# Optimization experiments

Hardware: AMD Instinct MI355X
Metric: run time of the kernel (lower is better)

## Reference

```python
import jax, jax.numpy as jnp
import numpy as np

B, H, S, D = 2, 16, 2048, 64

def setup_inputs() -> dict:
    key = jax.random.key(0)
    kq, kk, kv, km, ks = jax.random.split(key, 5)
    return {
        "query_input": jax.random.normal(kq, (B, H, S, D), dtype=jnp.float32),
        "key_input": jax.random.normal(kk, (B, H, S, D), dtype=jnp.float32),
        "value_input": jax.random.normal(kv, (B, H, S, D), dtype=jnp.float32),
        "query_mask": jnp.ones((B, 1, S, 1), dtype=jnp.float32),
        "key_mask": jax.random.uniform(km, (B, 1, 1, S), dtype=jnp.float32),
        "scale_factor": jax.random.normal(ks, (B, 1, 1, 1), dtype=jnp.float32),
        "dropout": 0,
    }

def reference(query_input, key_input, value_input, query_mask, key_mask, scale_factor, dropout):
    # qk = q @ k^T  -> [B, H, S, S]
    qk = jnp.einsum("bhqd,bhkd->bhqk", query_input, key_input)
    scaled_qk = qk * scale_factor                      # elementwise per-batch scale
    softmax_qk = jax.nn.softmax(scaled_qk, axis=-1)
    masked = softmax_qk * key_mask                     # post-softmax multiplicative mask
    # dropout with p=0 is the identity (deterministic baseline)
    output = jnp.einsum("bhqk,bhkd->bhqd", masked, value_input)
    return output
```

## Files before the change

kernel.cpp:

```cpp
#include <hip/hip_runtime.h>
#include <hip/hip_bf16.h>
#include <stdint.h>

#define BB 2
#define HH 16
#define SS 2048
#define DD 64
constexpr int BH = BB * HH;
constexpr int NT = SS / 64;
constexpr int QB = 16;

typedef _Float16 f16_t;
typedef f16_t f16x8 __attribute__((ext_vector_type(8)));
typedef float f32x4 __attribute__((ext_vector_type(4)));

__device__ __forceinline__ uint32_t pkf16(float a, float b) {
    return __builtin_bit_cast(uint32_t, __builtin_amdgcn_cvt_pkrtz(a, b));
}

__global__ __launch_bounds__(256)
void prepack(const float* __restrict__ Kg, const float* __restrict__ Vg,
             const float* __restrict__ Mg, f16_t* __restrict__ Kp,
             f16_t* __restrict__ Vp)
{
    __shared__ float Vs[64][65];
    const int bh = blockIdx.x % BH;
    const int kt = blockIdx.x / BH;
    const int b  = bh / HH;
    const int t  = threadIdx.x;
    const size_t gbase = (size_t)bh * SS * DD + (size_t)kt * 64 * DD;
    const size_t tbase = ((size_t)bh * NT + kt) * 4096;

    for (int c = t; c < 512; c += 256) {
        const int row = c >> 3, j = c & 7;
        const float* kp = Kg + gbase + (size_t)row * DD + j * 8;
        float4 a = *(const float4*)kp;
        float4 d = *(const float4*)(kp + 4);
        uint4 w = make_uint4(pkf16(a.x, a.y), pkf16(a.z, a.w),
                             pkf16(d.x, d.y), pkf16(d.z, d.w));
        *(uint4*)&Kp[tbase + (size_t)row * 64 + ((j ^ (row & 7)) * 8)] = w;
    }

    for (int c = t; c < 1024; c += 256) {
        const int key = c >> 4, dc = (c & 15) * 4;
        float4 v = *(const float4*)(Vg + gbase + (size_t)key * DD + dc);
        const float m = Mg[(size_t)b * SS + kt * 64 + key];
        Vs[key][dc + 0] = v.x * m;
        Vs[key][dc + 1] = v.y * m;
        Vs[key][dc + 2] = v.z * m;
        Vs[key][dc + 3] = v.w * m;
    }
    __syncthreads();

    for (int c = t; c < 512; c += 256) {
        const int dr = c >> 3, j = c & 7;
        float v0 = Vs[j * 8 + 0][dr], v1 = Vs[j * 8 + 1][dr];
        float v2 = Vs[j * 8 + 2][dr], v3 = Vs[j * 8 + 3][dr];
        float v4 = Vs[j * 8 + 4][dr], v5 = Vs[j * 8 + 5][dr];
        float v6 = Vs[j * 8 + 6][dr], v7 = Vs[j * 8 + 7][dr];
        uint4 w = make_uint4(pkf16(v0, v1), pkf16(v2, v3),
                             pkf16(v4, v5), pkf16(v6, v7));
        *(uint4*)&Vp[tbase + (size_t)dr * 64 + ((j ^ (dr & 7)) * 8)] = w;
    }
}

__global__ __launch_bounds__(512)
void fattn8(const float* __restrict__ Qg, const f16_t* __restrict__ Kp,
            const f16_t* __restrict__ Vp, const float* __restrict__ Sg,
            float* __restrict__ Og)
{
    __shared__ __align__(16) f16_t Kt[2][4096];
    __shared__ __align__(16) f16_t Vt[3][4096];
    __shared__ __align__(16) f16_t Pt[8][16][72];

    const int bh   = blockIdx.x % BH;
    const int qt   = blockIdx.x / BH;
    const int b    = bh / HH;
    const int tid  = threadIdx.x;
    const int wave = tid >> 6;
    const int lane = tid & 63;
    const int l16  = lane & 15;
    const int quad = lane >> 4;

    const float sc = Sg[b] * 1.44269504088896340736f;
    const size_t base = (size_t)bh * SS * DD;
    const size_t tb0  = (size_t)bh * NT * 4096;
    const int q0 = qt * 128 + wave * 16;

    auto stage = [&](int kt, int kbuf, int vbuf) {
        const f16_t* ks = Kp + tb0 + (size_t)kt * 4096 + tid * 8;
        const f16_t* vs = Vp + tb0 + (size_t)kt * 4096 + tid * 8;
        __builtin_amdgcn_global_load_lds(
            (const __attribute__((address_space(1))) void*)ks,
            (__attribute__((address_space(3))) void*)&Kt[kbuf][wave * 512],
            16, 0, 0);
        __builtin_amdgcn_global_load_lds(
            (const __attribute__((address_space(1))) void*)vs,
            (__attribute__((address_space(3))) void*)&Vt[vbuf][wave * 512],
            16, 0, 0);
    };

    stage(0, 0, 0);

    f16x8 qf[2];
    {
        const float* qp = Qg + base + (size_t)(q0 + l16) * DD + quad * 8;
#pragma unroll
        for (int kc = 0; kc < 2; ++kc) {
            float4 a  = *(const float4*)(qp + kc * 32);
            float4 b4 = *(const float4*)(qp + kc * 32 + 4);
            f16x8 f;
            f[0] = (f16_t)(a.x * sc);  f[1] = (f16_t)(a.y * sc);
            f[2] = (f16_t)(a.z * sc);  f[3] = (f16_t)(a.w * sc);
            f[4] = (f16_t)(b4.x * sc); f[5] = (f16_t)(b4.y * sc);
            f[6] = (f16_t)(b4.z * sc); f[7] = (f16_t)(b4.w * sc);
            qf[kc] = f;
        }
    }

    f32x4 Ot[4];
#pragma unroll
    for (int mt = 0; mt < 4; ++mt) Ot[mt] = f32x4{0.f, 0.f, 0.f, 0.f};
    float m_run = -1e30f, l_run = 0.0f;

    const int swz = (l16 & 7) << 3;

    int vcur = 0;
    for (int kt = 0; kt < NT; ++kt) {
        const int kcur = kt & 1;
        const int vnxt = (vcur == 2) ? 0 : vcur + 1;
        if (kt + 1 < NT) {
            stage(kt + 1, kcur ^ 1, vnxt);
            asm volatile("s_waitcnt vmcnt(2)" ::: "memory");
        } else {
            asm volatile("s_waitcnt vmcnt(0)" ::: "memory");
        }
        __builtin_amdgcn_s_barrier();

        __builtin_amdgcn_s_setprio(1);
        f32x4 Sfr[4];
#pragma unroll
        for (int mt = 0; mt < 4; ++mt) {
            f32x4 acc = f32x4{0.f, 0.f, 0.f, 0.f};
#pragma unroll
            for (int kc = 0; kc < 2; ++kc) {
                const int off = (mt * 16 + l16) * 64 + ((kc * 32 + quad * 8) ^ swz);
                f16x8 kh = *(const f16x8*)&Kt[kcur][off];
                acc = __builtin_amdgcn_mfma_f32_16x16x32_f16(kh, qf[kc], acc, 0, 0, 0);
            }
            Sfr[mt] = acc;
        }

        if (kt > 0) {
            const int vprv = (vcur == 0) ? 2 : vcur - 1;
#pragma unroll
            for (int kc = 0; kc < 2; ++kc) {
                f16x8 pf = *(const f16x8*)&Pt[wave][l16][kc * 32 + quad * 8];
#pragma unroll
                for (int mt = 0; mt < 4; ++mt) {
                    const int off = (mt * 16 + l16) * 64 + ((kc * 32 + quad * 8) ^ swz);
                    f16x8 vf = *(const f16x8*)&Vt[vprv][off];
                    Ot[mt] = __builtin_amdgcn_mfma_f32_16x16x32_f16(vf, pf, Ot[mt], 0, 0, 0);
                }
            }
        }
        __builtin_amdgcn_s_setprio(0);

        float a0 = fmaxf(fmaxf(Sfr[0][0], Sfr[0][1]), Sfr[0][2]);
        float b0 = fmaxf(fmaxf(Sfr[1][0], Sfr[1][1]), Sfr[1][2]);
        a0 = fmaxf(fmaxf(a0, Sfr[0][3]), Sfr[2][0]);
        b0 = fmaxf(fmaxf(b0, Sfr[1][3]), Sfr[2][1]);
        a0 = fmaxf(fmaxf(a0, Sfr[2][2]), Sfr[3][0]);
        b0 = fmaxf(fmaxf(b0, Sfr[2][3]), Sfr[3][1]);
        a0 = fmaxf(fmaxf(a0, Sfr[3][2]), Sfr[3][3]);
        float mx = fmaxf(a0, b0);
        mx = fmaxf(mx, __shfl_xor(mx, 16));
        mx = fmaxf(mx, __shfl_xor(mx, 32));

        if (__any(mx > m_run + 8.0f)) {
            const float mnew  = fmaxf(m_run, mx);
            const float alpha = __builtin_amdgcn_exp2f(m_run - mnew);
            m_run = mnew;
            l_run *= alpha;
#pragma unroll
            for (int mt = 0; mt < 4; ++mt) Ot[mt] *= alpha;
        }

        float ps[4][4];
#pragma unroll
        for (int mt = 0; mt < 4; ++mt)
#pragma unroll
            for (int r = 0; r < 4; ++r)
                ps[mt][r] = __builtin_amdgcn_exp2f(Sfr[mt][r] - m_run);

        float s0 = (ps[0][0] + ps[0][1]) + (ps[0][2] + ps[0][3]);
        float s1 = (ps[1][0] + ps[1][1]) + (ps[1][2] + ps[1][3]);
        float s2 = (ps[2][0] + ps[2][1]) + (ps[2][2] + ps[2][3]);
        float s3 = (ps[3][0] + ps[3][1]) + (ps[3][2] + ps[3][3]);
        float rs = (s0 + s1) + (s2 + s3);
        rs += __shfl_xor(rs, 16);
        rs += __shfl_xor(rs, 32);
        l_run += rs;

#pragma unroll
        for (int mt = 0; mt < 4; ++mt) {
            uint2 w = make_uint2(pkf16(ps[mt][0], ps[mt][1]),
                                 pkf16(ps[mt][2], ps[mt][3]));
            *(uint2*)&Pt[wave][l16][mt * 16 + quad * 4] = w;
        }

        __builtin_amdgcn_s_barrier();
        vcur = vnxt;
    }

    {
        const int vprv = (vcur == 0) ? 2 : vcur - 1;
#pragma unroll
        for (int kc = 0; kc < 2; ++kc) {
            f16x8 pf = *(const f16x8*)&Pt[wave][l16][kc * 32 + quad * 8];
#pragma unroll
            for (int mt = 0; mt < 4; ++mt) {
                const int off = (mt * 16 + l16) * 64 + ((kc * 32 + quad * 8) ^ swz);
                f16x8 vf = *(const f16x8*)&Vt[vprv][off];
                Ot[mt] = __builtin_amdgcn_mfma_f32_16x16x32_f16(vf, pf, Ot[mt], 0, 0, 0);
            }
        }
    }

    const float inv = 1.0f / l_run;
    float* op = Og + base + (size_t)(q0 + l16) * DD + quad * 4;
#pragma unroll
    for (int mt = 0; mt < 4; ++mt) {
#pragma unroll
        for (int r = 0; r < 4; ++r)
            op[mt * 16 + r] = Ot[mt][r] * inv;
    }
}

__global__ __launch_bounds__(512)
void fattn6(const float* __restrict__ Qg, const float* __restrict__ Kg,
            const float* __restrict__ Vg, const float* __restrict__ Mg,
            const float* __restrict__ Sg, float* __restrict__ Og)
{
    __shared__ __align__(16) f16_t Kh_lds[64][72];
    __shared__ __align__(16) f16_t Vt_lds[64][72];
    __shared__ __align__(16) f16_t Pt_lds[8][16][72];
    __shared__ float msk_lds[SS];

    const int bh   = blockIdx.x % BH;
    const int qt   = blockIdx.x / BH;
    const int b    = bh / HH;
    const int tid  = threadIdx.x;
    const int wave = tid >> 6;
    const int lane = tid & 63;
    const int l16  = lane & 15;
    const int quad = lane >> 4;

    const float sc = Sg[b] * 1.44269504088896340736f;
    const size_t base = (size_t)bh * SS * DD;
    const int q0 = qt * 128 + wave * 16;

    for (int i = tid; i < SS; i += 512) msk_lds[i] = Mg[(size_t)b * SS + i];

    f16x8 qf[2];
    {
        const float* qp = Qg + base + (size_t)(q0 + l16) * DD + quad * 8;
#pragma unroll
        for (int kc = 0; kc < 2; ++kc) {
            float4 a  = *(const float4*)(qp + kc * 32);
            float4 b4 = *(const float4*)(qp + kc * 32 + 4);
            f16x8 f;
            f[0] = (f16_t)(a.x * sc);  f[1] = (f16_t)(a.y * sc);
            f[2] = (f16_t)(a.z * sc);  f[3] = (f16_t)(a.w * sc);
            f[4] = (f16_t)(b4.x * sc); f[5] = (f16_t)(b4.y * sc);
            f[6] = (f16_t)(b4.z * sc); f[7] = (f16_t)(b4.w * sc);
            qf[kc] = f;
        }
    }

    f32x4 Ot[4];
#pragma unroll
    for (int mt = 0; mt < 4; ++mt) Ot[mt] = f32x4{0.f, 0.f, 0.f, 0.f};
    float m_run = -1e30f, l_run = 0.0f;

    const int krow = tid >> 3;
    const int kc8  = (tid & 7) * 8;
    const int vd   = tid & 63;
    const int vk0  = (tid >> 6) * 8;

    for (int kt = 0; kt < NT; ++kt) {
        __syncthreads();
        {
            const float* kp = Kg + base + (size_t)(kt * 64 + krow) * DD + kc8;
            float4 a0 = *(const float4*)(kp);
            float4 a1 = *(const float4*)(kp + 4);
            uint4 w = make_uint4(pkf16(a0.x, a0.y), pkf16(a0.z, a0.w),
                                 pkf16(a1.x, a1.y), pkf16(a1.z, a1.w));
            *(uint4*)&Kh_lds[krow][kc8] = w;
        }
        {
            const float* vp = Vg + base + (size_t)(kt * 64 + vk0) * DD + vd;
            const float* mp = &msk_lds[kt * 64 + vk0];
            float v0 = vp[0 * DD] * mp[0], v1 = vp[1 * DD] * mp[1];
            float v2 = vp[2 * DD] * mp[2], v3 = vp[3 * DD] * mp[3];
            float v4 = vp[4 * DD] * mp[4], v5 = vp[5 * DD] * mp[5];
            float v6 = vp[6 * DD] * mp[6], v7 = vp[7 * DD] * mp[7];
            uint4 w = make_uint4(pkf16(v0, v1), pkf16(v2, v3),
                                 pkf16(v4, v5), pkf16(v6, v7));
            *(uint4*)&Vt_lds[vd][vk0] = w;
        }
        __syncthreads();

        f32x4 Sfr[4];
#pragma unroll
        for (int mt = 0; mt < 4; ++mt) {
            f32x4 acc = f32x4{0.f, 0.f, 0.f, 0.f};
#pragma unroll
            for (int kc = 0; kc < 2; ++kc) {
                f16x8 kh = *(const f16x8*)&Kh_lds[mt * 16 + l16][kc * 32 + quad * 8];
                acc = __builtin_amdgcn_mfma_f32_16x16x32_f16(kh, qf[kc], acc, 0, 0, 0);
            }
            Sfr[mt] = acc;
        }

        float mx = Sfr[0][0];
#pragma unroll
        for (int mt = 0; mt < 4; ++mt)
#pragma unroll
            for (int r = 0; r < 4; ++r) mx = fmaxf(mx, Sfr[mt][r]);
        mx = fmaxf(mx, __shfl_xor(mx, 16));
        mx = fmaxf(mx, __shfl_xor(mx, 32));

        if (__any(mx > m_run)) {
            const float mnew  = fmaxf(m_run, mx);
            const float alpha = exp2f(m_run - mnew);
            m_run = mnew;
            l_run *= alpha;
#pragma unroll
            for (int mt = 0; mt < 4; ++mt) Ot[mt] *= alpha;
        }

        float ps[4][4];
        float rs = 0.0f;
#pragma unroll
        for (int mt = 0; mt < 4; ++mt)
#pragma unroll
            for (int r = 0; r < 4; ++r) {
                ps[mt][r] = exp2f(Sfr[mt][r] - m_run);
                rs += ps[mt][r];
            }
        rs += __shfl_xor(rs, 16);
        rs += __shfl_xor(rs, 32);
        l_run += rs;

#pragma unroll
        for (int mt = 0; mt < 4; ++mt) {
            uint2 w = make_uint2(pkf16(ps[mt][0], ps[mt][1]),
                                 pkf16(ps[mt][2], ps[mt][3]));
            *(uint2*)&Pt_lds[wave][l16][mt * 16 + quad * 4] = w;
        }

#pragma unroll
        for (int kc = 0; kc < 2; ++kc) {
            f16x8 pf = *(const f16x8*)&Pt_lds[wave][l16][kc * 32 + quad * 8];
#pragma unroll
            for (int mt = 0; mt < 4; ++mt) {
                f16x8 vf = *(const f16x8*)&Vt_lds[mt * 16 + l16][kc * 32 + quad * 8];
                Ot[mt] = __builtin_amdgcn_mfma_f32_16x16x32_f16(vf, pf, Ot[mt], 0, 0, 0);
            }
        }
    }

    const float inv = 1.0f / l_run;
    float* op = Og + base + (size_t)(q0 + l16) * DD + quad * 4;
#pragma unroll
    for (int mt = 0; mt < 4; ++mt) {
#pragma unroll
        for (int r = 0; r < 4; ++r)
            op[mt * 16 + r] = Ot[mt][r] * inv;
    }
}

extern "C" void kernel_launch(void* const* d_in, const int* in_sizes, int n_in,
                              void* d_out, int out_size, void* d_ws, size_t ws_size,
                              hipStream_t stream) {
    const float* Qg = (const float*)d_in[0];
    const float* Kg = (const float*)d_in[1];
    const float* Vg = (const float*)d_in[2];
    const float* Mg = (const float*)d_in[4];
    const float* Sg = (const float*)d_in[5];
    float* Og = (float*)d_out;

    const size_t kv_elems = (size_t)BH * SS * DD;
    const size_t need = 2 * kv_elems * sizeof(f16_t);

    if (d_ws != nullptr && ws_size >= need) {
        f16_t* Kp = (f16_t*)d_ws;
        f16_t* Vp = Kp + kv_elems;
        prepack<<<dim3(BH * NT), dim3(256), 0, stream>>>(Kg, Vg, Mg, Kp, Vp);
        fattn8<<<dim3(BH * QB), dim3(512), 0, stream>>>(Qg, Kp, Vp, Sg, Og);
    } else {
        fattn6<<<dim3(BH * QB), dim3(512), 0, stream>>>(Qg, Kg, Vg, Mg, Sg, Og);
    }
}
```

Measured before the change: 154.7 us.

## Compute softmax row sums with an MFMA against ones and defer max shuffles

The per-tile row-sum of probabilities moves off the VALU and cross-lane shuffles onto the matrix unit: an extra MFMA multiplies a vector of ones by the P fragment, so the denominator accumulates alongside the output. The max reduction now uses fused three-input max operations, and its cross-lane shuffles run only when a lane's local max exceeds the threshold, which triggers a rescale. This removes two shuffles and the add tree from every iteration. In exchange it adds two MFMAs per tile, and the denominator is now summed from the f16-rounded probabilities rather than the fp32 values.

```diff
diff --git a/kernel.cpp b/kernel.cpp
--- a/kernel.cpp
+++ b/kernel.cpp
@@ -16,6 +16,9 @@
 
 __device__ __forceinline__ uint32_t pkf16(float a, float b) {
     return __builtin_bit_cast(uint32_t, __builtin_amdgcn_cvt_pkrtz(a, b));
+}
+__device__ __forceinline__ float fmax3(float a, float b, float c) {
+    return fmaxf(fmaxf(a, b), c);
 }
 
 __global__ __launch_bounds__(256)
@@ -65,9 +68,9 @@
 }
 
 __global__ __launch_bounds__(512)
-void fattn8(const float* __restrict__ Qg, const f16_t* __restrict__ Kp,
-            const f16_t* __restrict__ Vp, const float* __restrict__ Sg,
-            float* __restrict__ Og)
+void fattn10(const float* __restrict__ Qg, const f16_t* __restrict__ Kp,
+             const f16_t* __restrict__ Vp, const float* __restrict__ Sg,
+             float* __restrict__ Og)
 {
     __shared__ __align__(16) f16_t Kt[2][4096];
     __shared__ __align__(16) f16_t Vt[3][4096];
@@ -118,10 +121,15 @@
         }
     }
 
+    f16x8 ones;
+#pragma unroll
+    for (int i = 0; i < 8; ++i) ones[i] = (f16_t)1.0f;
+
     f32x4 Ot[4];
 #pragma unroll
     for (int mt = 0; mt < 4; ++mt) Ot[mt] = f32x4{0.f, 0.f, 0.f, 0.f};
-    float m_run = -1e30f, l_run = 0.0f;
+    f32x4 Osum = f32x4{0.f, 0.f, 0.f, 0.f};
+    float m_run = -1e30f;
 
     const int swz = (l16 & 7) << 3;
 
@@ -162,28 +170,29 @@
                     f16x8 vf = *(const f16x8*)&Vt[vprv][off];
                     Ot[mt] = __builtin_amdgcn_mfma_f32_16x16x32_f16(vf, pf, Ot[mt], 0, 0, 0);
                 }
+                Osum = __builtin_amdgcn_mfma_f32_16x16x32_f16(ones, pf, Osum, 0, 0, 0);
             }
         }
         __builtin_amdgcn_s_setprio(0);
 
-        float a0 = fmaxf(fmaxf(Sfr[0][0], Sfr[0][1]), Sfr[0][2]);
-        float b0 = fmaxf(fmaxf(Sfr[1][0], Sfr[1][1]), Sfr[1][2]);
-        a0 = fmaxf(fmaxf(a0, Sfr[0][3]), Sfr[2][0]);
-        b0 = fmaxf(fmaxf(b0, Sfr[1][3]), Sfr[2][1]);
-        a0 = fmaxf(fmaxf(a0, Sfr[2][2]), Sfr[3][0]);
-        b0 = fmaxf(fmaxf(b0, Sfr[2][3]), Sfr[3][1]);
-        a0 = fmaxf(fmaxf(a0, Sfr[3][2]), Sfr[3][3]);
-        float mx = fmaxf(a0, b0);
-        mx = fmaxf(mx, __shfl_xor(mx, 16));
-        mx = fmaxf(mx, __shfl_xor(mx, 32));
-
-        if (__any(mx > m_run + 8.0f)) {
-            const float mnew  = fmaxf(m_run, mx);
+        float g0 = fmax3(Sfr[0][0], Sfr[0][1], Sfr[0][2]);
+        float g1 = fmax3(Sfr[0][3], Sfr[1][0], Sfr[1][1]);
+        float g2 = fmax3(Sfr[1][2], Sfr[1][3], Sfr[2][0]);
+        float g3 = fmax3(Sfr[2][1], Sfr[2][2], Sfr[2][3]);
+        float g4 = fmax3(Sfr[3][0], Sfr[3][1], Sfr[3][2]);
+        float h0 = fmax3(g0, g1, Sfr[3][3]);
+        float h1 = fmax3(g2, g3, g4);
+        const float lmax = fmaxf(h0, h1);
+
+        if (__any(lmax > m_run + 8.0f)) {
+            float mxq = fmaxf(lmax, __shfl_xor(lmax, 16));
+            mxq = fmaxf(mxq, __shfl_xor(mxq, 32));
+            const float mnew  = fmaxf(m_run, mxq);
             const float alpha = __builtin_amdgcn_exp2f(m_run - mnew);
             m_run = mnew;
-            l_run *= alpha;
 #pragma unroll
             for (int mt = 0; mt < 4; ++mt) Ot[mt] *= alpha;
+            Osum *= alpha;
         }
 
         float ps[4][4];
@@ -192,15 +201,6 @@
 #pragma unroll
             for (int r = 0; r < 4; ++r)
                 ps[mt][r] = __builtin_amdgcn_exp2f(Sfr[mt][r] - m_run);
-
-        float s0 = (ps[0][0] + ps[0][1]) + (ps[0][2] + ps[0][3]);
-        float s1 = (ps[1][0] + ps[1][1]) + (ps[1][2] + ps[1][3]);
-        float s2 = (ps[2][0] + ps[2][1]) + (ps[2][2] + ps[2][3]);
-        float s3 = (ps[3][0] + ps[3][1]) + (ps[3][2] + ps[3][3]);
-        float rs = (s0 + s1) + (s2 + s3);
-        rs += __shfl_xor(rs, 16);
-        rs += __shfl_xor(rs, 32);
-        l_run += rs;
 
 #pragma unroll
         for (int mt = 0; mt < 4; ++mt) {
@@ -224,10 +224,11 @@
                 f16x8 vf = *(const f16x8*)&Vt[vprv][off];
                 Ot[mt] = __builtin_amdgcn_mfma_f32_16x16x32_f16(vf, pf, Ot[mt], 0, 0, 0);
             }
-        }
-    }
-
-    const float inv = 1.0f / l_run;
+            Osum = __builtin_amdgcn_mfma_f32_16x16x32_f16(ones, pf, Osum, 0, 0, 0);
+        }
+    }
+
+    const float inv = 1.0f / Osum[0];
     float* op = Og + base + (size_t)(q0 + l16) * DD + quad * 4;
 #pragma unroll
     for (int mt = 0; mt < 4; ++mt) {
@@ -398,7 +399,7 @@
         f16_t* Kp = (f16_t*)d_ws;
         f16_t* Vp = Kp + kv_elems;
         prepack<<<dim3(BH * NT), dim3(256), 0, stream>>>(Kg, Vg, Mg, Kp, Vp);
-        fattn8<<<dim3(BH * QB), dim3(512), 0, stream>>>(Qg, Kp, Vp, Sg, Og);
+        fattn10<<<dim3(BH * QB), dim3(512), 0, stream>>>(Qg, Kp, Vp, Sg, Og);
     } else {
         fattn6<<<dim3(BH * QB), dim3(512), 0, stream>>>(Qg, Kg, Vg, Mg, Sg, Og);
     }
```

Result: faster. 146.6 us (-5.2%).
